# Kernel optimization log

Hardware: AMD Instinct MI355X
Metric: run time of the kernel (lower is better)

## Reference

```python
import jax, jax.numpy as jnp
import numpy as np

B, T, C, H, Wimg = 16, 6, 4, 420, 312
PH, PW = 14, 12
E = 768
GH, GW = H // PH, Wimg // PW  # 30, 26 -> 780 patches
N_VALID = 390


def setup_inputs() -> dict:
    key = jax.random.key(0)
    kx, kw, kb = jax.random.split(key, 3)
    x = jax.random.normal(kx, (B, T, C, H, Wimg), dtype=jnp.float32)
    W = jax.random.normal(kw, (E, C, PH, PW), dtype=jnp.float32) * 0.02
    b = jax.random.normal(kb, (E,), dtype=jnp.float32) * 0.02
    # static patch mask: keep half the patches (unique, sorted indices like torch.nonzero)
    rng = np.random.default_rng(0)
    valid = np.sort(rng.choice(GH * GW, size=N_VALID, replace=False)).astype(np.int32)
    return {"x": x, "W": W, "b": b, "valid_indices": jnp.asarray(valid)}


def reference(x, W, b, valid_indices):
    Bv, Tv, Cv, Hv, Wv = x.shape
    Ev, _, ph, pw = W.shape
    gh, gw = Hv // ph, Wv // pw
    # non-overlapping stride=kernel conv == patchify + GEMM
    xp = x.reshape(Bv * Tv, Cv, gh, ph, gw, pw)
    out = jnp.einsum('ncipjq,ecpq->nije', xp, W) + b  # [B*T, gh, gw, E]
    out = out.reshape(Bv, Tv, gh * gw, Ev)            # [B, T, n_patches, E]
    return out[:, :, valid_indices, :]                # [B, T, n_valid, E]
```

## Files before the change

### kernel.cpp

```cpp
#include <hip/hip_runtime.h>

#define M_TOT 37440
#define N_E   768
#define K_TOT 672
#define NV    390
#define GWID  26
#define PHh   14
#define PWw   12
#define IMW   312
#define CSTRIDE 131040
#define NSTRIDE 524160

typedef short bf16x8 __attribute__((ext_vector_type(8)));
typedef float f32x4  __attribute__((ext_vector_type(4)));
typedef unsigned short u16;
typedef u16 u16x4 __attribute__((ext_vector_type(4)));
typedef u16 u16x8 __attribute__((ext_vector_type(8)));

#define A_WS_BYTES 50319360u
#define W_WS_ELEMS 516096
#define WS_NEEDED (A_WS_BYTES + W_WS_ELEMS*2)

#define NBLK_A 8190
#define NBLK_W 252

static __device__ __forceinline__ u16 f2bf(float f) {
  unsigned u = __builtin_bit_cast(unsigned, f);
  u = (u + 0x7FFFu + ((u >> 16) & 1u)) >> 16;
  return (u16)u;
}

#define GLOAD_LDS16(g, l) \
  __builtin_amdgcn_global_load_lds((const __attribute__((address_space(1))) void*)(g), \
                                   (__attribute__((address_space(3))) void*)(l), 16, 0, 0)

__global__ __launch_bounds__(256) void patchify(
    const float* __restrict__ x, const float* __restrict__ w,
    const int* __restrict__ valid, u16* __restrict__ A, u16* __restrict__ Wb) {
  const int bid = blockIdx.x;
  const int tid = threadIdx.x;
  if (bid < NBLK_A) {
    const int g  = bid * 256 + tid;
    const int m  = g / 56;
    const int rr = g - m * 56;
    const int nimg = m / NV;
    const int v    = m - nimg * NV;
    const int gidx = valid[v];
    const int gi = gidx / GWID, gj = gidx - gi * GWID;
    const int c  = rr / PHh,    p  = rr - c * PHh;
    const float* src = x + (size_t)nimg * NSTRIDE + (size_t)c * CSTRIDE
                         + (size_t)(gi * PHh + p) * IMW + gj * PWw;
    f32x4 f0 = *(const f32x4*)(src + 0);
    f32x4 f1 = *(const f32x4*)(src + 4);
    f32x4 f2 = *(const f32x4*)(src + 8);
    u16* dst = A + (size_t)m * K_TOT + rr * 12;
    u16x8 h01 = {f2bf(f0.x), f2bf(f0.y), f2bf(f0.z), f2bf(f0.w),
                 f2bf(f1.x), f2bf(f1.y), f2bf(f1.z), f2bf(f1.w)};
    u16x4 h2  = {f2bf(f2.x), f2bf(f2.y), f2bf(f2.z), f2bf(f2.w)};
    *(u16x8*)(dst + 0) = h01;
    *(u16x4*)(dst + 8) = h2;
  } else {
    const int g = (bid - NBLK_A) * 256 + tid;
    const float* src = w + (size_t)g * 8;
    f32x4 f0 = *(const f32x4*)(src + 0);
    f32x4 f1 = *(const f32x4*)(src + 4);
    u16x8 h = {f2bf(f0.x), f2bf(f0.y), f2bf(f0.z), f2bf(f0.w),
               f2bf(f1.x), f2bf(f1.y), f2bf(f1.z), f2bf(f1.w)};
    *(u16x8*)(Wb + (size_t)g * 8) = h;
  }
}

__global__ __launch_bounds__(256) void gemm_bf16(
    const u16* __restrict__ A, const u16* __restrict__ Bw,
    const float* __restrict__ bias, float* __restrict__ out) {
  __shared__ u16 Alds[128 * 96];
  __shared__ u16 Blds[128 * 96];
  char* AldsB = (char*)Alds;
  char* BldsB = (char*)Blds;

  const int tid  = threadIdx.x;
  const int lane = tid & 63;
  const int wid  = tid >> 6;
  const int wr   = wid >> 1, wc = wid & 1;
  const int lrow = lane & 15, lhi = lane >> 4;

  const int n0 = blockIdx.x * 128;
  const int m0 = blockIdx.y * 128;

  int aoff[6], boff[6];
  #pragma unroll
  for (int j = 0; j < 6; ++j) {
    const int ci  = wid * 384 + j * 64 + lane;
    const int row = ci / 12;
    const int c16 = ci - row * 12;
    int ar = m0 + row; if (ar >= M_TOT) ar = M_TOT - 1;
    aoff[j] = ar * K_TOT + c16 * 8;
    boff[j] = (n0 + row) * K_TOT + c16 * 8;
  }

  f32x4 acc[4][4];
  #pragma unroll
  for (int i = 0; i < 4; ++i)
    #pragma unroll
    for (int j = 0; j < 4; ++j)
      acc[i][j] = (f32x4){0.f, 0.f, 0.f, 0.f};

  for (int t = 0; t < 7; ++t) {
    const int kb = t * 96;
    #pragma unroll
    for (int j = 0; j < 6; ++j)
      GLOAD_LDS16(A + aoff[j] + kb, AldsB + (wid * 6 + j) * 1024);
    #pragma unroll
    for (int j = 0; j < 6; ++j)
      GLOAD_LDS16(Bw + boff[j] + kb, BldsB + (wid * 6 + j) * 1024);
    __syncthreads();

    #pragma unroll
    for (int kk = 0; kk < 3; ++kk) {
      bf16x8 a[4], b[4];
      #pragma unroll
      for (int i = 0; i < 4; ++i)
        a[i] = *(const bf16x8*)&Alds[(wr * 64 + i * 16 + lrow) * 96 + kk * 32 + lhi * 8];
      #pragma unroll
      for (int j = 0; j < 4; ++j)
        b[j] = *(const bf16x8*)&Blds[(wc * 64 + j * 16 + lrow) * 96 + kk * 32 + lhi * 8];
      #pragma unroll
      for (int i = 0; i < 4; ++i)
        #pragma unroll
        for (int j = 0; j < 4; ++j)
          acc[i][j] = __builtin_amdgcn_mfma_f32_16x16x32_bf16(a[i], b[j], acc[i][j], 0, 0, 0);
    }
    __syncthreads();
  }

  float bv[4];
  #pragma unroll
  for (int j = 0; j < 4; ++j)
    bv[j] = bias[n0 + wc * 64 + j * 16 + lrow];

  #pragma unroll
  for (int i = 0; i < 4; ++i) {
    const int mbase = m0 + wr * 64 + i * 16 + lhi * 4;
    #pragma unroll
    for (int j = 0; j < 4; ++j) {
      const int e = n0 + wc * 64 + j * 16 + lrow;
      float* op = out + (size_t)mbase * N_E + e;
      #pragma unroll
      for (int tt = 0; tt < 4; ++tt) {
        if (mbase + tt < M_TOT) op[(size_t)tt * N_E] = acc[i][j][tt] + bv[j];
      }
    }
  }
}

#define ROWB 104
__global__ __launch_bounds__(256) void patch_gemm_fused(
    const float* __restrict__ x, const float* __restrict__ w,
    const float* __restrict__ bias, const int* __restrict__ valid,
    float* __restrict__ out) {
  __shared__ u16 Alds[128 * ROWB];
  __shared__ u16 Blds[128 * ROWB];
  const int tid  = threadIdx.x;
  const int lane = tid & 63;
  const int wid  = tid >> 6;
  const int wr   = wid >> 1, wc = wid & 1;
  const int lrow = lane & 15, lhi = lane >> 4;
  const int m0 = blockIdx.x * 128;
  const int n0 = blockIdx.y * 128;
  const int arow = tid & 127;
  int m = m0 + arow;
  if (m >= M_TOT) m = M_TOT - 1;
  const int nimg = m / NV;
  const int v    = m - nimg * NV;
  const int g    = valid[v];
  const int gi   = g / GWID;
  const int gj   = g - gi * GWID;
  const float* xrow = x + (size_t)nimg * NSTRIDE + (size_t)(gi * PHh) * IMW + gj * PWw;
  const int half = tid >> 7;
  const float* wrow = w + (size_t)(n0 + arow) * K_TOT;
  f32x4 acc[4][4];
  #pragma unroll
  for (int i = 0; i < 4; ++i)
    #pragma unroll
    for (int j = 0; j < 4; ++j)
      acc[i][j] = (f32x4){0.f, 0.f, 0.f, 0.f};
  for (int t = 0; t < 7; ++t) {
    #pragma unroll
    for (int it = 0; it < 4; ++it) {
      const int run = half + it * 2;
      const int rr  = t * 8 + run;
      const int c   = rr / PHh;
      const int p   = rr - c * PHh;
      const float* src = xrow + (size_t)c * CSTRIDE + p * IMW;
      f32x4 f0 = *(const f32x4*)(src + 0);
      f32x4 f1 = *(const f32x4*)(src + 4);
      f32x4 f2 = *(const f32x4*)(src + 8);
      u16x4 h0 = {f2bf(f0.x), f2bf(f0.y), f2bf(f0.z), f2bf(f0.w)};
      u16x4 h1 = {f2bf(f1.x), f2bf(f1.y), f2bf(f1.z), f2bf(f1.w)};
      u16x4 h2 = {f2bf(f2.x), f2bf(f2.y), f2bf(f2.z), f2bf(f2.w)};
      u16* dst = &Alds[arow * ROWB + run * 12];
      *(u16x4*)(dst + 0) = h0;
      *(u16x4*)(dst + 4) = h1;
      *(u16x4*)(dst + 8) = h2;
    }
    #pragma unroll
    for (int i = 0; i < 6; ++i) {
      const int col = half * 48 + i * 8;
      const float* src = wrow + t * 96 + col;
      f32x4 f0 = *(const f32x4*)(src + 0);
      f32x4 f1 = *(const f32x4*)(src + 4);
      u16x8 h = {f2bf(f0.x), f2bf(f0.y), f2bf(f0.z), f2bf(f0.w),
                 f2bf(f1.x), f2bf(f1.y), f2bf(f1.z), f2bf(f1.w)};
      *(u16x8*)&Blds[arow * ROWB + col] = h;
    }
    __syncthreads();
    #pragma unroll
    for (int kk = 0; kk < 3; ++kk) {
      bf16x8 a[4], b[4];
      #pragma unroll
      for (int i = 0; i < 4; ++i)
        a[i] = *(const bf16x8*)&Alds[(wr * 64 + i * 16 + lrow) * ROWB + kk * 32 + lhi * 8];
      #pragma unroll
      for (int j = 0; j < 4; ++j)
        b[j] = *(const bf16x8*)&Blds[(wc * 64 + j * 16 + lrow) * ROWB + kk * 32 + lhi * 8];
      #pragma unroll
      for (int i = 0; i < 4; ++i)
        #pragma unroll
        for (int j = 0; j < 4; ++j)
          acc[i][j] = __builtin_amdgcn_mfma_f32_16x16x32_bf16(a[i], b[j], acc[i][j], 0, 0, 0);
    }
    __syncthreads();
  }
  float bv[4];
  #pragma unroll
  for (int j = 0; j < 4; ++j)
    bv[j] = bias[n0 + wc * 64 + j * 16 + lrow];
  #pragma unroll
  for (int i = 0; i < 4; ++i) {
    const int mbase = m0 + wr * 64 + i * 16 + lhi * 4;
    #pragma unroll
    for (int j = 0; j < 4; ++j) {
      const int e = n0 + wc * 64 + j * 16 + lrow;
      float* op = out + (size_t)mbase * N_E + e;
      #pragma unroll
      for (int tt = 0; tt < 4; ++tt) {
        if (mbase + tt < M_TOT) op[(size_t)tt * N_E] = acc[i][j][tt] + bv[j];
      }
    }
  }
}

extern "C" void kernel_launch(void* const* d_in, const int* in_sizes, int n_in,
                              void* d_out, int out_size, void* d_ws, size_t ws_size,
                              hipStream_t stream) {
  const float* x     = (const float*)d_in[0];
  const float* w     = (const float*)d_in[1];
  const float* b     = (const float*)d_in[2];
  const int*   valid = (const int*)d_in[3];
  float* out = (float*)d_out;

  if (ws_size >= (size_t)WS_NEEDED) {
    u16* Aws = (u16*)d_ws;
    u16* Wws = (u16*)((char*)d_ws + A_WS_BYTES);
    patchify<<<NBLK_A + NBLK_W, 256, 0, stream>>>(x, w, valid, Aws, Wws);
    dim3 grid(N_E / 128, (M_TOT + 127) / 128);
    gemm_bf16<<<grid, dim3(256), 0, stream>>>(Aws, Wws, b, out);
  } else {
    dim3 grid((M_TOT + 127) / 128, N_E / 128);
    patch_gemm_fused<<<grid, dim3(256), 0, stream>>>(x, w, b, valid, out);
  }
}
```

Baseline: 377.2 us.

## Double-buffer GEMM LDS stages with K-tile-major padded bf16 workspace

```diff
diff --git a/kernel.cpp b/kernel.cpp
--- a/kernel.cpp
+++ b/kernel.cpp
@@ -11,18 +11,20 @@
 #define CSTRIDE 131040
 #define NSTRIDE 524160
 
+#define NKT   7
+#define ROWP  104
+
 typedef short bf16x8 __attribute__((ext_vector_type(8)));
 typedef float f32x4  __attribute__((ext_vector_type(4)));
 typedef unsigned short u16;
 typedef u16 u16x4 __attribute__((ext_vector_type(4)));
-typedef u16 u16x8 __attribute__((ext_vector_type(8)));
-
-#define A_WS_BYTES 50319360u
-#define W_WS_ELEMS 516096
-#define WS_NEEDED (A_WS_BYTES + W_WS_ELEMS*2)
+
+#define A_PAD_BYTES 54512640u
+#define W_PAD_BYTES 1118208u
+#define WS_NEEDED   (A_PAD_BYTES + W_PAD_BYTES)
 
 #define NBLK_A 8190
-#define NBLK_W 252
+#define NBLK_W 168
 
 static __device__ __forceinline__ u16 f2bf(float f) {
   unsigned u = __builtin_bit_cast(unsigned, f);
@@ -36,13 +38,14 @@
 
 __global__ __launch_bounds__(256) void patchify(
     const float* __restrict__ x, const float* __restrict__ w,
-    const int* __restrict__ valid, u16* __restrict__ A, u16* __restrict__ Wb) {
+    const int* __restrict__ valid, u16* __restrict__ Ap, u16* __restrict__ Wp) {
   const int bid = blockIdx.x;
   const int tid = threadIdx.x;
   if (bid < NBLK_A) {
     const int g  = bid * 256 + tid;
     const int m  = g / 56;
     const int rr = g - m * 56;
+    const int t  = rr >> 3, run = rr & 7;
     const int nimg = m / NV;
     const int v    = m - nimg * NV;
     const int gidx = valid[v];
@@ -53,30 +56,36 @@
     f32x4 f0 = *(const f32x4*)(src + 0);
     f32x4 f1 = *(const f32x4*)(src + 4);
     f32x4 f2 = *(const f32x4*)(src + 8);
-    u16* dst = A + (size_t)m * K_TOT + rr * 12;
-    u16x8 h01 = {f2bf(f0.x), f2bf(f0.y), f2bf(f0.z), f2bf(f0.w),
-                 f2bf(f1.x), f2bf(f1.y), f2bf(f1.z), f2bf(f1.w)};
-    u16x4 h2  = {f2bf(f2.x), f2bf(f2.y), f2bf(f2.z), f2bf(f2.w)};
-    *(u16x8*)(dst + 0) = h01;
+    u16* dst = Ap + ((size_t)(t * M_TOT + m)) * ROWP + run * 12;
+    u16x4 h0 = {f2bf(f0.x), f2bf(f0.y), f2bf(f0.z), f2bf(f0.w)};
+    u16x4 h1 = {f2bf(f1.x), f2bf(f1.y), f2bf(f1.z), f2bf(f1.w)};
+    u16x4 h2 = {f2bf(f2.x), f2bf(f2.y), f2bf(f2.z), f2bf(f2.w)};
+    *(u16x4*)(dst + 0) = h0;
+    *(u16x4*)(dst + 4) = h1;
     *(u16x4*)(dst + 8) = h2;
   } else {
-    const int g = (bid - NBLK_A) * 256 + tid;
-    const float* src = w + (size_t)g * 8;
+    const int g  = (bid - NBLK_A) * 256 + tid;
+    const int n  = g / 56;
+    const int rr = g - n * 56;
+    const int t  = rr >> 3, run = rr & 7;
+    const float* src = w + (size_t)n * K_TOT + rr * 12;
     f32x4 f0 = *(const f32x4*)(src + 0);
     f32x4 f1 = *(const f32x4*)(src + 4);
-    u16x8 h = {f2bf(f0.x), f2bf(f0.y), f2bf(f0.z), f2bf(f0.w),
-               f2bf(f1.x), f2bf(f1.y), f2bf(f1.z), f2bf(f1.w)};
-    *(u16x8*)(Wb + (size_t)g * 8) = h;
+    f32x4 f2 = *(const f32x4*)(src + 8);
+    u16* dst = Wp + ((size_t)(t * N_E + n)) * ROWP + run * 12;
+    u16x4 h0 = {f2bf(f0.x), f2bf(f0.y), f2bf(f0.z), f2bf(f0.w)};
+    u16x4 h1 = {f2bf(f1.x), f2bf(f1.y), f2bf(f1.z), f2bf(f1.w)};
+    u16x4 h2 = {f2bf(f2.x), f2bf(f2.y), f2bf(f2.z), f2bf(f2.w)};
+    *(u16x4*)(dst + 0) = h0;
+    *(u16x4*)(dst + 4) = h1;
+    *(u16x4*)(dst + 8) = h2;
   }
 }
 
 __global__ __launch_bounds__(256) void gemm_bf16(
-    const u16* __restrict__ A, const u16* __restrict__ Bw,
+    const u16* __restrict__ Ap, const u16* __restrict__ Wp,
     const float* __restrict__ bias, float* __restrict__ out) {
-  __shared__ u16 Alds[128 * 96];
-  __shared__ u16 Blds[128 * 96];
-  char* AldsB = (char*)Alds;
-  char* BldsB = (char*)Blds;
+  __shared__ u16 lds[2][2][128 * ROWP];
 
   const int tid  = threadIdx.x;
   const int lane = tid & 63;
@@ -87,16 +96,23 @@
   const int n0 = blockIdx.x * 128;
   const int m0 = blockIdx.y * 128;
 
-  int aoff[6], boff[6];
-  #pragma unroll
-  for (int j = 0; j < 6; ++j) {
-    const int ci  = wid * 384 + j * 64 + lane;
-    const int row = ci / 12;
-    const int c16 = ci - row * 12;
-    int ar = m0 + row; if (ar >= M_TOT) ar = M_TOT - 1;
-    aoff[j] = ar * K_TOT + c16 * 8;
-    boff[j] = (n0 + row) * K_TOT + c16 * 8;
-  }
+  auto STAGE = [&](int t, int b) {
+    if (wid < 2) {
+      const u16* srcb = Ap + ((size_t)(t * M_TOT + m0)) * ROWP + lane * 8;
+      #pragma unroll
+      for (int j = 0; j < 13; ++j) {
+        const int c = wid * 13 + j;
+        GLOAD_LDS16(srcb + c * 512, (char*)&lds[b][0][0] + c * 1024);
+      }
+    } else {
+      const u16* srcb = Wp + ((size_t)(t * N_E + n0)) * ROWP + lane * 8;
+      #pragma unroll
+      for (int j = 0; j < 13; ++j) {
+        const int c = (wid - 2) * 13 + j;
+        GLOAD_LDS16(srcb + c * 512, (char*)&lds[b][1][0] + c * 1024);
+      }
+    }
+  };
 
   f32x4 acc[4][4];
   #pragma unroll
@@ -105,32 +121,35 @@
     for (int j = 0; j < 4; ++j)
       acc[i][j] = (f32x4){0.f, 0.f, 0.f, 0.f};
 
-  for (int t = 0; t < 7; ++t) {
-    const int kb = t * 96;
-    #pragma unroll
-    for (int j = 0; j < 6; ++j)
-      GLOAD_LDS16(A + aoff[j] + kb, AldsB + (wid * 6 + j) * 1024);
-    #pragma unroll
-    for (int j = 0; j < 6; ++j)
-      GLOAD_LDS16(Bw + boff[j] + kb, BldsB + (wid * 6 + j) * 1024);
-    __syncthreads();
+  STAGE(0, 0);
+
+  for (int t = 0; t < NKT; ++t) {
+    const int b = t & 1;
+    if (t < NKT - 1) {
+      STAGE(t + 1, b ^ 1);
+      asm volatile("s_waitcnt vmcnt(13)" ::: "memory");
+    } else {
+      asm volatile("s_waitcnt vmcnt(0)" ::: "memory");
+    }
+    __builtin_amdgcn_s_barrier();
 
     #pragma unroll
     for (int kk = 0; kk < 3; ++kk) {
-      bf16x8 a[4], b[4];
-      #pragma unroll
-      for (int i = 0; i < 4; ++i)
-        a[i] = *(const bf16x8*)&Alds[(wr * 64 + i * 16 + lrow) * 96 + kk * 32 + lhi * 8];
+      bf16x8 a[4], bfr[4];
+      #pragma unroll
+      for (int i = 0; i < 4; ++i)
+        a[i] = *(const bf16x8*)&lds[b][0][(wr * 64 + i * 16 + lrow) * ROWP + kk * 32 + lhi * 8];
       #pragma unroll
       for (int j = 0; j < 4; ++j)
-        b[j] = *(const bf16x8*)&Blds[(wc * 64 + j * 16 + lrow) * 96 + kk * 32 + lhi * 8];
+        bfr[j] = *(const bf16x8*)&lds[b][1][(wc * 64 + j * 16 + lrow) * ROWP + kk * 32 + lhi * 8];
       #pragma unroll
       for (int i = 0; i < 4; ++i)
         #pragma unroll
         for (int j = 0; j < 4; ++j)
-          acc[i][j] = __builtin_amdgcn_mfma_f32_16x16x32_bf16(a[i], b[j], acc[i][j], 0, 0, 0);
-    }
-    __syncthreads();
+          acc[i][j] = __builtin_amdgcn_mfma_f32_16x16x32_bf16(a[i], bfr[j], acc[i][j], 0, 0, 0);
+    }
+    asm volatile("" ::: "memory");
+    __builtin_amdgcn_s_barrier();
   }
 
   float bv[4];
@@ -209,9 +228,11 @@
       const float* src = wrow + t * 96 + col;
       f32x4 f0 = *(const f32x4*)(src + 0);
       f32x4 f1 = *(const f32x4*)(src + 4);
-      u16x8 h = {f2bf(f0.x), f2bf(f0.y), f2bf(f0.z), f2bf(f0.w),
-                 f2bf(f1.x), f2bf(f1.y), f2bf(f1.z), f2bf(f1.w)};
-      *(u16x8*)&Blds[arow * ROWB + col] = h;
+      u16x4 h0 = {f2bf(f0.x), f2bf(f0.y), f2bf(f0.z), f2bf(f0.w)};
+      u16x4 h1 = {f2bf(f1.x), f2bf(f1.y), f2bf(f1.z), f2bf(f1.w)};
+      u16* dst = &Blds[arow * ROWB + col];
+      *(u16x4*)(dst + 0) = h0;
+      *(u16x4*)(dst + 4) = h1;
     }
     __syncthreads();
     #pragma unroll
@@ -261,7 +282,7 @@
 
   if (ws_size >= (size_t)WS_NEEDED) {
     u16* Aws = (u16*)d_ws;
-    u16* Wws = (u16*)((char*)d_ws + A_WS_BYTES);
+    u16* Wws = (u16*)((char*)d_ws + A_PAD_BYTES);
     patchify<<<NBLK_A + NBLK_W, 256, 0, stream>>>(x, w, valid, Aws, Wws);
     dim3 grid(N_E / 128, (M_TOT + 127) / 128);
     gemm_bf16<<<grid, dim3(256), 0, stream>>>(Aws, Wws, b, out);
```

Measured after the change: 422.0 us. +11.9%, slower.
